# Kernel tuning notes

Hardware: AMD Instinct MI355X
Metric: run time of the kernel (lower is better)

## Reference

```python
import jax, jax.numpy as jnp
import numpy as np

N_ATOMS = 100000
N_PAIRS = 4000000
N_TYPES = 200
# atom_description columns
AT_NAME, RESNUM, CHAIN = 0, 1, 2
# atom_Properties columns
P_CHARGED, P_CHARGE, P_VIRTUAL, P_DIPOLE, P_RADIUS = 0, 1, 2, 3, 4
# atom-name hash codes (stand-ins for hashings.atom_hash entries)
PHE_RC, TYR_RC, ARG_CZ, ARG_ARG = 10, 11, 12, 13
TEMPERATURE = 298.0
CONSTANT = float(np.exp(-0.004314 * (TEMPERATURE - 273.0)))
DIELEC = 8.8
ION_CORR = 0.02 + 0.05 / 1.4  # Ionic_corrected
PAD = 999.0  # PADDING_INDEX
MAX_DISTANCE = 15.0
KON_APPROACH = 6.0
SOLV_DIELEC = 88.0
RAD10 = float(np.radians(10.0))
RAD30 = float(np.radians(30.0))
RAD150 = float(np.radians(150.0))
RAD180 = float(np.radians(180.0))


def setup_inputs() -> dict:
    key = jax.random.key(0)
    k = jax.random.split(key, 10)
    coords = jax.random.normal(k[0], (N_ATOMS, 3), jnp.float32) * 10.0
    partners = jax.random.normal(k[1], (N_ATOMS, 2, 3), jnp.float32) * 10.0
    at_name = jax.random.randint(k[2], (N_ATOMS,), 0, N_TYPES)
    resnum = jax.random.randint(k[3], (N_ATOMS,), 0, 500)
    chain = jax.random.randint(k[4], (N_ATOMS,), 0, 4)
    atom_description = jnp.stack([at_name, resnum, chain], axis=-1)
    atomPairs = jax.random.randint(k[5], (N_PAIRS, 2), 0, N_ATOMS)
    charged = jax.random.bernoulli(k[6], 0.4, (N_TYPES,)).astype(jnp.float32)
    charge = jax.random.choice(k[7], jnp.array([-1.0, -0.5, 0.5, 1.0], jnp.float32), (N_TYPES,)) * charged
    virtual = jax.random.bernoulli(k[8], 0.1, (N_TYPES,)).astype(jnp.float32)
    kd, kr = jax.random.split(k[9])
    dipole = jax.random.bernoulli(kd, 0.3, (N_TYPES,)).astype(jnp.float32)
    radius = jax.random.uniform(kr, (N_TYPES,), jnp.float32, 1.2, 2.2)
    atom_Properties = jnp.stack([charged, charge, virtual, dipole, radius], axis=-1)
    return {"coords": coords, "partners": partners, "atom_Properties": atom_Properties,
            "atom_description": atom_description, "atomPairs": atomPairs}


def _electro_energy(coords, partners, atom_Properties, atom_description, atomPairs):
    i = atomPairs[:, 0]
    j = atomPairs[:, 1]
    at1 = atom_description[i, AT_NAME]
    at2 = atom_description[j, AT_NAME]

    rc1 = (at1 == PHE_RC) | (at1 == TYR_RC)
    rc2 = (at2 == PHE_RC) | (at2 == TYR_RC)
    argInvolved = ((at1 == ARG_CZ) & ((at2 == ARG_CZ) | rc2)) | ((at2 == ARG_CZ) & ((at1 == ARG_CZ) | rc1))

    charged1 = atom_Properties[at1, P_CHARGED] == 1
    charged2 = atom_Properties[at2, P_CHARGED] == 1
    # NcpMask/CcpMask are all-False (calculate_helical_dipoles == False branch)
    is_charged = (charged1 & charged2) | argInvolved

    diff = coords[i] - coords[j]
    dist = jnp.sqrt(jnp.sum(diff * diff, axis=-1) + 1e-12)  # [P]

    same_res = (atom_description[i, RESNUM] != atom_description[j, RESNUM]) | \
               (atom_description[i, CHAIN] != atom_description[j, CHAIN])
    valid = is_charged & (dist <= MAX_DISTANCE) & same_res  # is_charged_mask & first_mask

    c1 = atom_Properties[at1, P_CHARGE]
    c2 = atom_Properties[at2, P_CHARGE]
    v1 = atom_Properties[at1, P_VIRTUAL] == 1
    v2 = atom_Properties[at2, P_VIRTUAL] == 1
    # hDipoleInvolved is all-False, so the helix-dipole term contributes 0
    charged_charged = valid & (c1 != 0) & (c2 != 0) & (c1 != PAD) & (c2 != PAD) & (~v1) & (~v2)

    # ---- ARG stacking term (plane angle between the two guanidinium/ring planes)
    pA0 = partners[i, 0]; pA1 = partners[i, 1]; cA = coords[i]
    pB0 = partners[j, 0]; pB1 = partners[j, 1]; cB = coords[j]
    n1 = jnp.cross(pA0 - cA, pA1 - cA)
    n2 = jnp.cross(pB0 - cB, pB1 - cB)
    nn1 = jnp.sqrt(jnp.sum(n1 * n1, axis=-1) + 1e-12)
    nn2 = jnp.sqrt(jnp.sum(n2 * n2, axis=-1) + 1e-12)
    m = (nn1 > 1e-6) & (nn2 > 1e-6)
    cosang = jnp.clip(jnp.sum(n1 * n2, axis=-1) / (nn1 * nn2), -0.999999, 0.999999)
    ang = jnp.arccos(cosang)
    ang_bad = ((ang > RAD30) & (ang < RAD150)) | (dist < 3.9) | (dist > 4.3) | (~m)
    arg_mask = valid & argInvolved & (~ang_bad)

    dsafe = jnp.maximum(dist, 1e-6)
    argEpss = 332.0 / (dsafe * DIELEC * CONSTANT)
    temp_d = 3.0 + jnp.abs(dist - 4.1)
    angCorr = dist > RAD150  # faithful to source: distance compared against radians(150)
    corr_ang = jnp.where(angCorr,
                         jnp.maximum((RAD180 - ang) / RAD10, 1.0),
                         jnp.maximum(dist / RAD10, 1.0))
    arg_arg = (at1 == ARG_ARG) & (at2 == ARG_ARG)
    c1e = jnp.ones_like(dist)
    c2e = jnp.where(arg_arg, -1.0, -0.5)
    vk = jnp.sqrt(200.0 * jnp.abs(c1e * c2e) * ION_CORR / TEMPERATURE)
    argE = (1.0 / corr_ang) * c1e * c2e * argEpss * jnp.exp(-temp_d * vk) / (temp_d * temp_d)

    # ---- kon (association-rate electrostatics) term, inter-chain non-dipole charges
    dip1 = atom_Properties[at1, P_DIPOLE] == 0
    dip2 = atom_Properties[at2, P_DIPOLE] == 0
    inter_chain = atom_description[i, CHAIN] != atom_description[j, CHAIN]
    kon_mask = charged_charged & dip1 & dip2 & inter_chain
    sum_radii = atom_Properties[at1, P_RADIUS] + atom_Properties[at2, P_RADIUS] - 0.09
    dd = jnp.maximum(dist, sum_radii)
    temp_kon = jnp.maximum(dd + dd * dd / 30.0, KON_APPROACH)
    IONSTRENGTH = 0.05
    k_on = jnp.sqrt(200.0 * jnp.abs(c1) * jnp.abs(c2) * IONSTRENGTH / TEMPERATURE)
    firstNumber = 332.0 * c1 * c2 / (SOLV_DIELEC * temp_kon * CONSTANT)
    secondNumber = jnp.exp(-k_on * (temp_kon - KON_APPROACH))
    thirdSecond = 1.0 + k_on * KON_APPROACH
    konE = 0.5 * firstNumber * secondNumber / thirdSecond

    zero = jnp.zeros_like(dist)
    virtual_energy = jnp.where(arg_mask, argE, zero) + jnp.where(kon_mask, konE, zero)
    return virtual_energy  # [P], zero at pairs the torch code compacted away


def reference(coords, partners, atom_Properties, atom_description, atomPairs):
    return _electro_energy(coords, partners, atom_Properties, atom_description, atomPairs)
```

## Files before the change

### kernel.cpp

```cpp
#include <hip/hip_runtime.h>
#include <math.h>

namespace {
constexpr int   NTYPES   = 200;
constexpr float RAD10_   = 0.17453292519943295f;
constexpr float RAD30_   = 0.52359877559829882f;
constexpr float RAD150_  = 2.6179938779914944f;
constexpr float RAD180_  = 3.14159265358979323f;
constexpr float CONST_T  = 0.89776110649108887f;

constexpr float ARG_K   = 42.0237329f;
constexpr float KON_K   = 2.10118664f;
constexpr float KON_SQK = 0.18318583f;
constexpr float VK_AA   = 0.19337050f;
constexpr float VK_MIX  = 0.13673360f;

constexpr unsigned RC_B   = 1u << 19;
constexpr unsigned CZ_B   = 1u << 20;
constexpr unsigned AA_B   = 1u << 21;
constexpr unsigned CHG_B  = 1u << 22;
constexpr unsigned VIRT_B = 1u << 23;
constexpr unsigned DIP0_B = 1u << 24;
constexpr unsigned MAG_B  = 1u << 25;
constexpr unsigned SGN_B  = 1u << 26;
constexpr unsigned RESCH_M = 0x7FF00u;
constexpr unsigned CHAIN_M = 0x300u;

constexpr int MAX_FILT_WORDS = 3200;
}

typedef int   i4v __attribute__((ext_vector_type(4)));
typedef float f2v __attribute__((ext_vector_type(2)));

__global__ __launch_bounds__(256) void prep_all(
    const float* __restrict__ coords,
    const float* __restrict__ props,
    const int*   __restrict__ desc,
    float4*      __restrict__ rec,
    unsigned*    __restrict__ filt,
    int nwords, int natoms)
{
    const int idx = blockIdx.x * blockDim.x + threadIdx.x;
    bool interesting = false;
    if (idx < natoms) {
        const int at  = desc[3 * idx];
        const int res = desc[3 * idx + 1];
        const int ch  = desc[3 * idx + 2];
        unsigned bits = (unsigned)at | ((unsigned)ch << 8) | ((unsigned)res << 10);
        if ((at == 10) | (at == 11))       bits |= RC_B;
        if (at == 12)                      bits |= CZ_B;
        if (at == 13)                      bits |= AA_B;
        const float c = props[5 * at + 1];
        if (props[5 * at + 0] == 1.0f)     bits |= CHG_B;
        if (props[5 * at + 2] == 1.0f)     bits |= VIRT_B;
        if (props[5 * at + 3] == 0.0f)     bits |= DIP0_B;
        if (fabsf(c) == 1.0f)              bits |= MAG_B;
        if (c < 0.0f)                      bits |= SGN_B;
        rec[idx] = make_float4(coords[3 * idx], coords[3 * idx + 1],
                               coords[3 * idx + 2], __uint_as_float(bits));
        interesting = ((bits & CHG_B) != 0) | ((bits & (CZ_B | RC_B)) != 0);
    }
    const unsigned long long m = __ballot(interesting);
    const unsigned lane = threadIdx.x & 63u;
    if ((lane & 31u) == 0u) {
        const int w = idx >> 5;
        if (w < nwords) filt[w] = (unsigned)(m >> lane);
    }
}

__device__ __forceinline__ float pe(
    const float4 A, const float4 B, int i, int j,
    const float* __restrict__ partners)
{
    const unsigned ba = __float_as_uint(A.w);
    const unsigned bb = __float_as_uint(B.w);

    const float dx = A.x - B.x, dy = A.y - B.y, dz = A.z - B.z;
    const float dist = sqrtf(dx * dx + dy * dy + dz * dz + 1e-12f);
    const bool diff_res = ((ba ^ bb) & RESCH_M) != 0;
    if (!((dist <= 15.0f) & diff_res)) return 0.0f;

    float energy = 0.0f;

    const bool czA = (ba & CZ_B) != 0, czB = (bb & CZ_B) != 0;
    const bool rcA = (ba & RC_B) != 0, rcB = (bb & RC_B) != 0;
    const bool argInv = (czA & (czB | rcB)) | (czB & (czA | rcA));
    if (argInv && (dist >= 3.9f) && (dist <= 4.3f)) {
        const float a0x = partners[6 * i],     a0y = partners[6 * i + 1], a0z = partners[6 * i + 2];
        const float a1x = partners[6 * i + 3], a1y = partners[6 * i + 4], a1z = partners[6 * i + 5];
        const float b0x = partners[6 * j],     b0y = partners[6 * j + 1], b0z = partners[6 * j + 2];
        const float b1x = partners[6 * j + 3], b1y = partners[6 * j + 4], b1z = partners[6 * j + 5];
        const float u1x = a0x - A.x, u1y = a0y - A.y, u1z = a0z - A.z;
        const float v1x = a1x - A.x, v1y = a1y - A.y, v1z = a1z - A.z;
        const float n1x = u1y * v1z - u1z * v1y;
        const float n1y = u1z * v1x - u1x * v1z;
        const float n1z = u1x * v1y - u1y * v1x;
        const float u2x = b0x - B.x, u2y = b0y - B.y, u2z = b0z - B.z;
        const float v2x = b1x - B.x, v2y = b1y - B.y, v2z = b1z - B.z;
        const float n2x = u2y * v2z - u2z * v2y;
        const float n2y = u2z * v2x - u2x * v2z;
        const float n2z = u2x * v2y - u2y * v2x;
        const float nn1 = sqrtf(n1x * n1x + n1y * n1y + n1z * n1z + 1e-12f);
        const float nn2 = sqrtf(n2x * n2x + n2y * n2y + n2z * n2z + 1e-12f);
        const bool  m = (nn1 > 1e-6f) & (nn2 > 1e-6f);
        float cosang = (n1x * n2x + n1y * n2y + n1z * n2z) / (nn1 * nn2);
        cosang = fminf(fmaxf(cosang, -0.999999f), 0.999999f);
        const float ang = acosf(cosang);
        const bool ang_mid_bad = (ang > RAD30_) & (ang < RAD150_);
        if (m & !ang_mid_bad) {
            const float temp_d = 3.0f + fabsf(dist - 4.1f);
            const float corr = fmaxf((RAD180_ - ang) * (1.0f / RAD10_), 1.0f);
            const bool  arg_arg = ((ba & bb & AA_B) != 0);
            const float c2e = arg_arg ? -1.0f : -0.5f;
            const float vk  = arg_arg ? VK_AA : VK_MIX;
            energy += c2e * ARG_K * expf(-temp_d * vk) /
                      (corr * dist * temp_d * temp_d);
        }
    }

    const bool kon = ((ba & bb & CHG_B) != 0) &
                     (((ba | bb) & VIRT_B) == 0) &
                     ((ba & bb & DIP0_B) != 0) &
                     (((ba ^ bb) & CHAIN_M) != 0);
    if (kon) {
        const float tk = fmaxf(dist + dist * dist * (1.0f / 30.0f), 6.0f);
        const int ms = (int)((ba >> 25) & 1u) + (int)((bb >> 25) & 1u);
        const float mag  = (ms == 0) ? 0.25f : ((ms == 1) ? 0.5f : 1.0f);
        const float k_on = KON_SQK * ((ms == 0) ? 0.5f : ((ms == 1) ? 0.70710678f : 1.0f));
        const float e = KON_K * mag * expf(-k_on * (tk - 6.0f)) /
                        (tk * (1.0f + 6.0f * k_on));
        energy += (((ba ^ bb) & SGN_B) != 0) ? -e : e;
    }
    return energy;
}

__global__ __launch_bounds__(256, 6) void electro_k11(
    const float4*   __restrict__ rec,
    const unsigned* __restrict__ filtg,
    const float*    __restrict__ partners,
    const int*      __restrict__ pairs_raw,
    float*          __restrict__ out,
    int n, int nwords, int tiles)
{
    __shared__ unsigned sfilt[MAX_FILT_WORDS];
    {
        const uint4* fsrc = reinterpret_cast<const uint4*>(filtg);
        const int nv = nwords >> 2;
        for (int t = threadIdx.x; t < nv; t += 256) {
            const uint4 v = fsrc[t];
            sfilt[4 * t]     = v.x;  sfilt[4 * t + 1] = v.y;
            sfilt[4 * t + 2] = v.z;  sfilt[4 * t + 3] = v.w;
        }
        for (int t = (nv << 2) + threadIdx.x; t < nwords; t += 256)
            sfilt[t] = filtg[t];
    }
    __syncthreads();

    const int tid = (int)threadIdx.x;

    auto load_tile = [&](int tile) -> i4v {
        const int p = (tile << 9) + 2 * tid;
        if (p + 1 < n)
            return __builtin_nontemporal_load(
                reinterpret_cast<const i4v*>(pairs_raw + 2 * p));
        i4v r = (i4v)0;
        if (p < n) { r.x = pairs_raw[2 * p]; r.y = pairs_raw[2 * p + 1]; }
        return r;
    };

    int tile = blockIdx.x;
    if (tile >= tiles) return;
    i4v cur = load_tile(tile);

    while (true) {
        const int next = tile + gridDim.x;
        i4v nxt = (i4v)0;
        if (next < tiles) nxt = load_tile(next);

        const int p0 = (tile << 9) + 2 * tid;
        const int i0 = cur.x, j0 = cur.y, i1 = cur.z, j1 = cur.w;

        const bool f0 = (((sfilt[i0 >> 5] >> (i0 & 31)) & (sfilt[j0 >> 5] >> (j0 & 31))) & 1u) != 0;
        const bool f1 = (((sfilt[i1 >> 5] >> (i1 & 31)) & (sfilt[j1 >> 5] >> (j1 & 31))) & 1u) != 0;

        const int a0 = f0 ? i0 : 0, b0 = f0 ? j0 : 0;
        const int a1 = f1 ? i1 : 0, b1 = f1 ? j1 : 0;

        const float4 A0 = rec[a0];
        const float4 B0 = rec[b0];
        const float4 A1 = rec[a1];
        const float4 B1 = rec[b1];

        const float e0 = f0 ? pe(A0, B0, i0, j0, partners) : 0.0f;
        const float e1 = f1 ? pe(A1, B1, i1, j1, partners) : 0.0f;

        if (p0 + 1 < n) {
            f2v r; r.x = e0; r.y = e1;
            __builtin_nontemporal_store(r, reinterpret_cast<f2v*>(out + p0));
        } else if (p0 < n) {
            out[p0] = e0;
        }

        if (next >= tiles) break;
        tile = next;
        cur  = nxt;
    }
}

__global__ __launch_bounds__(256) void electro_fallback(
    const float* __restrict__ coords, const float* __restrict__ partners,
    const float* __restrict__ props, const int* __restrict__ desc,
    const int2* __restrict__ pairs, float* __restrict__ out, int n)
{
    __shared__ float sp[NTYPES * 5];
    for (int t = threadIdx.x; t < NTYPES * 5; t += blockDim.x) sp[t] = props[t];
    __syncthreads();
    const int stride = gridDim.x * blockDim.x;
    for (int p = blockIdx.x * blockDim.x + threadIdx.x; p < n; p += stride) {
        const int2 ij = pairs[p];
        const int i = ij.x, j = ij.y;
        const int at1 = desc[3 * i], at2 = desc[3 * j];
        const bool rc1 = (at1 == 10) | (at1 == 11);
        const bool rc2 = (at2 == 10) | (at2 == 11);
        const bool argInv = ((at1 == 12) & ((at2 == 12) | rc2)) |
                            ((at2 == 12) & ((at1 == 12) | rc1));
        const float* p1 = &sp[5 * at1];
        const float* p2 = &sp[5 * at2];
        const bool is_charged = ((p1[0] == 1.0f) & (p2[0] == 1.0f)) | argInv;
        float energy = 0.0f;
        if (is_charged) {
            const int res1 = desc[3 * i + 1], ch1 = desc[3 * i + 2];
            const int res2 = desc[3 * j + 1], ch2 = desc[3 * j + 2];
            const float ax = coords[3 * i], ay = coords[3 * i + 1], az = coords[3 * i + 2];
            const float bx = coords[3 * j], by = coords[3 * j + 1], bz = coords[3 * j + 2];
            const float dx = ax - bx, dy = ay - by, dz = az - bz;
            const float dist = sqrtf(dx * dx + dy * dy + dz * dz + 1e-12f);
            const bool diff_res = (res1 != res2) | (ch1 != ch2);
            if ((dist <= 15.0f) & diff_res) {
                if (argInv && (dist >= 3.9f) && (dist <= 4.3f)) {
                    const float a0x = partners[6*i],   a0y = partners[6*i+1], a0z = partners[6*i+2];
                    const float a1x = partners[6*i+3], a1y = partners[6*i+4], a1z = partners[6*i+5];
                    const float b0x = partners[6*j],   b0y = partners[6*j+1], b0z = partners[6*j+2];
                    const float b1x = partners[6*j+3], b1y = partners[6*j+4], b1z = partners[6*j+5];
                    const float u1x=a0x-ax,u1y=a0y-ay,u1z=a0z-az;
                    const float v1x=a1x-ax,v1y=a1y-ay,v1z=a1z-az;
                    const float n1x=u1y*v1z-u1z*v1y, n1y=u1z*v1x-u1x*v1z, n1z=u1x*v1y-u1y*v1x;
                    const float u2x=b0x-bx,u2y=b0y-by,u2z=b0z-bz;
                    const float v2x=b1x-bx,v2y=b1y-by,v2z=b1z-bz;
                    const float n2x=u2y*v2z-u2z*v2y, n2y=u2z*v2x-u2x*v2z, n2z=u2x*v2y-u2y*v2x;
                    const float nn1 = sqrtf(n1x*n1x+n1y*n1y+n1z*n1z+1e-12f);
                    const float nn2 = sqrtf(n2x*n2x+n2y*n2y+n2z*n2z+1e-12f);
                    const bool m = (nn1 > 1e-6f) & (nn2 > 1e-6f);
                    float cosang = (n1x*n2x+n1y*n2y+n1z*n2z)/(nn1*nn2);
                    cosang = fminf(fmaxf(cosang, -0.999999f), 0.999999f);
                    const float ang = acosf(cosang);
                    const bool ang_mid_bad = (ang > RAD30_) & (ang < RAD150_);
                    if (m & !ang_mid_bad) {
                        const float dsafe = fmaxf(dist, 1e-6f);
                        const float argEpss = 332.0f / (dsafe * 8.8f * CONST_T);
                        const float temp_d = 3.0f + fabsf(dist - 4.1f);
                        const float corr_ang = (dist > RAD150_)
                            ? fmaxf((RAD180_ - ang) / RAD10_, 1.0f)
                            : fmaxf(dist / RAD10_, 1.0f);
                        const bool arg_arg = (at1 == 13) & (at2 == 13);
                        const float c2e = arg_arg ? -1.0f : -0.5f;
                        const float vk = sqrtf(200.0f * fabsf(c2e) * (0.02f + 0.05f/1.4f) / 298.0f);
                        energy += (1.0f/corr_ang)*c2e*argEpss*expf(-temp_d*vk)/(temp_d*temp_d);
                    }
                }
                const float c1 = p1[1], c2 = p2[1];
                const bool cc = (c1 != 0.0f) & (c2 != 0.0f) &
                                (p1[2] != 1.0f) & (p2[2] != 1.0f);
                const bool kon_mask = cc & (p1[3] == 0.0f) & (p2[3] == 0.0f) & (ch1 != ch2);
                if (kon_mask) {
                    const float sum_radii = p1[4] + p2[4] - 0.09f;
                    const float dd = fmaxf(dist, sum_radii);
                    const float tk = fmaxf(dd + dd*dd*(1.0f/30.0f), 6.0f);
                    const float k_on = sqrtf(200.0f*fabsf(c1)*fabsf(c2)*0.05f/298.0f);
                    const float first = 332.0f*c1*c2/(88.0f*tk*CONST_T);
                    const float second = expf(-k_on*(tk-6.0f));
                    const float third = 1.0f + k_on*6.0f;
                    energy += 0.5f*first*second/third;
                }
            }
        }
        out[p] = energy;
    }
}

extern "C" void kernel_launch(void* const* d_in, const int* in_sizes, int n_in,
                              void* d_out, int out_size, void* d_ws, size_t ws_size,
                              hipStream_t stream) {
    const float* coords   = (const float*)d_in[0];
    const float* partners = (const float*)d_in[1];
    const float* props    = (const float*)d_in[2];
    const int*   desc     = (const int*)d_in[3];
    const int*   pairs_i  = (const int*)d_in[4];
    float*       out      = (float*)d_out;

    const int natoms = in_sizes[0] / 3;
    const int n      = in_sizes[4] / 2;
    const int nwords = (natoms + 31) / 32;

    const size_t rec_bytes  = (size_t)natoms * sizeof(float4);
    const size_t filt_off   = (rec_bytes + 255) & ~(size_t)255;
    const size_t need_bytes = filt_off + (size_t)nwords * sizeof(unsigned);

    if (ws_size >= need_bytes && nwords <= MAX_FILT_WORDS) {
        float4*   rec  = (float4*)d_ws;
        unsigned* filt = (unsigned*)((char*)d_ws + filt_off);
        prep_all<<<(natoms + 255) / 256, 256, 0, stream>>>(
            coords, props, desc, rec, filt, nwords, natoms);
        const int tiles = (n + 511) / 512;
        int grid = tiles < 2560 ? tiles : 2560;
        electro_k11<<<grid, 256, 0, stream>>>(rec, filt, partners, pairs_i,
                                              out, n, nwords, tiles);
    } else {
        const int block = 256;
        int grid = (n + block - 1) / block;
        if (grid > 2048) grid = 2048;
        electro_fallback<<<grid, block, 0, stream>>>(coords, partners, props,
                                                     desc, (const int2*)pairs_i, out, n);
    }
}
```

Baseline: 30.48 us.

## Process four pairs per thread and tighten atom filter to kon-capable charges

```diff
diff --git a/kernel.cpp b/kernel.cpp
--- a/kernel.cpp
+++ b/kernel.cpp
@@ -30,7 +30,7 @@
 }
 
 typedef int   i4v __attribute__((ext_vector_type(4)));
-typedef float f2v __attribute__((ext_vector_type(2)));
+typedef float f4v __attribute__((ext_vector_type(4)));
 
 __global__ __launch_bounds__(256) void prep_all(
     const float* __restrict__ coords,
@@ -58,7 +58,9 @@
         if (c < 0.0f)                      bits |= SGN_B;
         rec[idx] = make_float4(coords[3 * idx], coords[3 * idx + 1],
                                coords[3 * idx + 2], __uint_as_float(bits));
-        interesting = ((bits & CHG_B) != 0) | ((bits & (CZ_B | RC_B)) != 0);
+        const bool kon_cap = ((bits & CHG_B) != 0) & ((bits & VIRT_B) == 0) &
+                             ((bits & DIP0_B) != 0);
+        interesting = kon_cap | ((bits & (CZ_B | RC_B)) != 0);
     }
     const unsigned long long m = __ballot(interesting);
     const unsigned lane = threadIdx.x & 63u;
@@ -134,7 +136,7 @@
     return energy;
 }
 
-__global__ __launch_bounds__(256, 6) void electro_k11(
+__global__ __launch_bounds__(256, 6) void electro_k12(
     const float4*   __restrict__ rec,
     const unsigned* __restrict__ filtg,
     const float*    __restrict__ partners,
@@ -158,52 +160,66 @@
 
     const int tid = (int)threadIdx.x;
 
-    auto load_tile = [&](int tile) -> i4v {
-        const int p = (tile << 9) + 2 * tid;
-        if (p + 1 < n)
-            return __builtin_nontemporal_load(
-                reinterpret_cast<const i4v*>(pairs_raw + 2 * p));
-        i4v r = (i4v)0;
-        if (p < n) { r.x = pairs_raw[2 * p]; r.y = pairs_raw[2 * p + 1]; }
-        return r;
+    auto load_tile = [&](int tile, i4v& a, i4v& b) {
+        const int p = (tile << 10) + 4 * tid;
+        if (p + 3 < n) {
+            a = __builtin_nontemporal_load(reinterpret_cast<const i4v*>(pairs_raw + 2 * p));
+            b = __builtin_nontemporal_load(reinterpret_cast<const i4v*>(pairs_raw + 2 * p + 4));
+        } else {
+            a = (i4v)0; b = (i4v)0;
+            if (p     < n) { a.x = pairs_raw[2*p];     a.y = pairs_raw[2*p + 1]; }
+            if (p + 1 < n) { a.z = pairs_raw[2*p + 2]; a.w = pairs_raw[2*p + 3]; }
+            if (p + 2 < n) { b.x = pairs_raw[2*p + 4]; b.y = pairs_raw[2*p + 5]; }
+        }
     };
 
     int tile = blockIdx.x;
     if (tile >= tiles) return;
-    i4v cur = load_tile(tile);
+    i4v curA, curB;
+    load_tile(tile, curA, curB);
 
     while (true) {
         const int next = tile + gridDim.x;
-        i4v nxt = (i4v)0;
-        if (next < tiles) nxt = load_tile(next);
-
-        const int p0 = (tile << 9) + 2 * tid;
-        const int i0 = cur.x, j0 = cur.y, i1 = cur.z, j1 = cur.w;
+        i4v nxtA = (i4v)0, nxtB = (i4v)0;
+        if (next < tiles) load_tile(next, nxtA, nxtB);
+
+        const int p0 = (tile << 10) + 4 * tid;
+        const int i0 = curA.x, j0 = curA.y, i1 = curA.z, j1 = curA.w;
+        const int i2 = curB.x, j2 = curB.y, i3 = curB.z, j3 = curB.w;
 
         const bool f0 = (((sfilt[i0 >> 5] >> (i0 & 31)) & (sfilt[j0 >> 5] >> (j0 & 31))) & 1u) != 0;
         const bool f1 = (((sfilt[i1 >> 5] >> (i1 & 31)) & (sfilt[j1 >> 5] >> (j1 & 31))) & 1u) != 0;
+        const bool f2 = (((sfilt[i2 >> 5] >> (i2 & 31)) & (sfilt[j2 >> 5] >> (j2 & 31))) & 1u) != 0;
+        const bool f3 = (((sfilt[i3 >> 5] >> (i3 & 31)) & (sfilt[j3 >> 5] >> (j3 & 31))) & 1u) != 0;
 
         const int a0 = f0 ? i0 : 0, b0 = f0 ? j0 : 0;
         const int a1 = f1 ? i1 : 0, b1 = f1 ? j1 : 0;
-
-        const float4 A0 = rec[a0];
-        const float4 B0 = rec[b0];
-        const float4 A1 = rec[a1];
-        const float4 B1 = rec[b1];
+        const int a2 = f2 ? i2 : 0, b2 = f2 ? j2 : 0;
+        const int a3 = f3 ? i3 : 0, b3 = f3 ? j3 : 0;
+
+        const float4 A0 = rec[a0];  const float4 B0 = rec[b0];
+        const float4 A1 = rec[a1];  const float4 B1 = rec[b1];
+        const float4 A2 = rec[a2];  const float4 B2 = rec[b2];
+        const float4 A3 = rec[a3];  const float4 B3 = rec[b3];
 
         const float e0 = f0 ? pe(A0, B0, i0, j0, partners) : 0.0f;
         const float e1 = f1 ? pe(A1, B1, i1, j1, partners) : 0.0f;
-
-        if (p0 + 1 < n) {
-            f2v r; r.x = e0; r.y = e1;
-            __builtin_nontemporal_store(r, reinterpret_cast<f2v*>(out + p0));
-        } else if (p0 < n) {
-            out[p0] = e0;
+        const float e2 = f2 ? pe(A2, B2, i2, j2, partners) : 0.0f;
+        const float e3 = f3 ? pe(A3, B3, i3, j3, partners) : 0.0f;
+
+        if (p0 + 3 < n) {
+            f4v r; r.x = e0; r.y = e1; r.z = e2; r.w = e3;
+            __builtin_nontemporal_store(r, reinterpret_cast<f4v*>(out + p0));
+        } else {
+            if (p0     < n) out[p0]     = e0;
+            if (p0 + 1 < n) out[p0 + 1] = e1;
+            if (p0 + 2 < n) out[p0 + 2] = e2;
         }
 
         if (next >= tiles) break;
         tile = next;
-        cur  = nxt;
+        curA = nxtA;
+        curB = nxtB;
     }
 }
 
@@ -311,9 +327,9 @@
         unsigned* filt = (unsigned*)((char*)d_ws + filt_off);
         prep_all<<<(natoms + 255) / 256, 256, 0, stream>>>(
             coords, props, desc, rec, filt, nwords, natoms);
-        const int tiles = (n + 511) / 512;
+        const int tiles = (n + 1023) / 1024;
         int grid = tiles < 2560 ? tiles : 2560;
-        electro_k11<<<grid, 256, 0, stream>>>(rec, filt, partners, pairs_i,
+        electro_k12<<<grid, 256, 0, stream>>>(rec, filt, partners, pairs_i,
                                               out, n, nwords, tiles);
     } else {
         const int block = 256;
```

Result: slower. 34.31 us (+12.6%).
